# Optimization experiments

Hardware: AMD Instinct MI355X
Metric: run time of the kernel (lower is better)

## Reference

```python
import jax, jax.numpy as jnp
import numpy as np

NUM_HEADS = 16
HEAD_DIM = 64
NEG_INF = -1000000000.0


def rotary_embedding(x, seq_len, head_dim):
    # x: (batch, seq, heads, head_dim)
    positions = jnp.arange(seq_len)
    dim_pairs = jnp.arange(0, head_dim, 2)
    freqs = 1.0 / 10000.0 ** (dim_pairs / head_dim)
    angles = positions[:, None] * freqs[None, :]          # (seq, head_dim/2)
    cos = jnp.cos(angles)[:, None, :]                     # (seq, 1, head_dim/2) -> broadcast over heads
    sin = jnp.sin(angles)[:, None, :]
    x1 = x[..., ::2]
    x2 = x[..., 1::2]
    out1 = x1 * cos - x2 * sin
    out2 = x1 * sin + x2 * cos
    return jnp.stack([out1, out2], axis=-1).reshape(x.shape)


def setup_inputs() -> dict:
    key = jax.random.key(0)
    k1, k2, k3 = jax.random.split(key, 3)
    batch, seq_len, embed_dim = 2, 2048, 1024
    x = jax.random.normal(k1, (batch, seq_len, embed_dim), dtype=jnp.float32)
    W_qkv = jax.random.normal(k2, (embed_dim, 3 * NUM_HEADS * HEAD_DIM), dtype=jnp.float32) * 0.02
    W_out = jax.random.normal(k3, (NUM_HEADS * HEAD_DIM, embed_dim), dtype=jnp.float32) * 0.02
    return {"x": x, "W_qkv": W_qkv, "W_out": W_out}


def reference(x, W_qkv, W_out):
    batch, seq_len, embed_dim = x.shape
    qkv = jnp.einsum('bse,ef->bsf', x, W_qkv)
    qkv = qkv.reshape(batch, seq_len, 3, NUM_HEADS, HEAD_DIM)
    q, k, v = qkv[:, :, 0], qkv[:, :, 1], qkv[:, :, 2]
    q = rotary_embedding(q, seq_len, HEAD_DIM)
    k = rotary_embedding(k, seq_len, HEAD_DIM)
    scale = 1.0 / jnp.sqrt(jnp.asarray(HEAD_DIM, dtype=x.dtype))
    scores = jnp.einsum('bqhd,bkhd->bhqk', q, k) * scale   # (B,H,S,S)
    mask = jnp.tril(jnp.ones((seq_len, seq_len), dtype=bool))[None, None, :, :]
    scores = jnp.where(mask, scores, NEG_INF)
    weights = jax.nn.softmax(scores, axis=-1)
    out = jnp.einsum('bhqk,bkhd->bqhd', weights, v)
    out = out.reshape(batch, seq_len, NUM_HEADS * HEAD_DIM)
    return jnp.einsum('bsf,fe->bse', out, W_out)
```

## Files before the change

kernel.cpp:

```cpp
#include <hip/hip_runtime.h>
#include <hip/hip_bf16.h>

typedef __attribute__((ext_vector_type(8))) short short8;
typedef __attribute__((ext_vector_type(4))) float float4v;

__global__ __launch_bounds__(256) void cvt_f32_bf16(
    const float* __restrict__ in, __hip_bfloat16* __restrict__ out, int n4) {
  const int i = blockIdx.x * 256 + threadIdx.x;
  if (i >= n4) return;
  const float4 v = *(const float4*)(in + (size_t)i * 4);
  __hip_bfloat16 o[4];
  o[0] = __float2bfloat16(v.x); o[1] = __float2bfloat16(v.y);
  o[2] = __float2bfloat16(v.z); o[3] = __float2bfloat16(v.w);
  *(uint2*)(out + (size_t)i * 4) = *(const uint2*)o;
}

__global__ __launch_bounds__(256) void transpose_f32_bf16(
    const float* __restrict__ in, __hip_bfloat16* __restrict__ out,
    int R, int C) {
  __shared__ __hip_bfloat16 tile[32][33];
  const int c0 = blockIdx.x * 32, r0 = blockIdx.y * 32;
  const int tx = threadIdx.x & 31, ty = threadIdx.x >> 5;
  #pragma unroll
  for (int i = ty; i < 32; i += 8)
    tile[i][tx] = __float2bfloat16(in[(size_t)(r0 + i) * C + (c0 + tx)]);
  __syncthreads();
  #pragma unroll
  for (int i = ty; i < 32; i += 8)
    out[(size_t)(c0 + i) * R + (r0 + tx)] = tile[tx][i];
}

template <typename OutT>
__global__ __launch_bounds__(256) void gemm_bt(
    const __hip_bfloat16* __restrict__ A,
    const __hip_bfloat16* __restrict__ Bt,
    OutT* __restrict__ C,
    int M, int N, int K) {
  __shared__ __hip_bfloat16 lA[128][64];
  __shared__ __hip_bfloat16 lB[128][64];
  const int t = threadIdx.x;
  const int lane = t & 63, wave = t >> 6;
  const int quad = lane >> 4, ln = lane & 15;
  const int m0 = blockIdx.y * 128, n0 = blockIdx.x * 128;
  const int wm = (wave >> 1) * 64, wn = (wave & 1) * 64;
  const int srow = lane >> 3;
  const int schunk = ((lane & 7) ^ srow) * 8;

  float4v acc[4][4];
  #pragma unroll
  for (int i = 0; i < 4; ++i)
    #pragma unroll
    for (int j = 0; j < 4; ++j)
      acc[i][j] = (float4v){0.f, 0.f, 0.f, 0.f};

  for (int kt = 0; kt < K; kt += 64) {
    __syncthreads();
    #pragma unroll
    for (int q = 0; q < 4; ++q) {
      const int rbase = wave * 32 + q * 8;
      __builtin_amdgcn_global_load_lds(
          (const __attribute__((address_space(1))) void*)
              (A + (size_t)(m0 + rbase + srow) * K + kt + schunk),
          (__attribute__((address_space(3))) void*)&lA[rbase][0], 16, 0, 0);
      __builtin_amdgcn_global_load_lds(
          (const __attribute__((address_space(1))) void*)
              (Bt + (size_t)(n0 + rbase + srow) * K + kt + schunk),
          (__attribute__((address_space(3))) void*)&lB[rbase][0], 16, 0, 0);
    }
    __syncthreads();
    #pragma unroll
    for (int step = 0; step < 2; ++step) {
      short8 af[4], bf[4];
      #pragma unroll
      for (int i = 0; i < 4; ++i)
        af[i] = *(const short8*)&lA[wm + i * 16 + ln][((step * 4 + quad) ^ (ln & 7)) * 8];
      #pragma unroll
      for (int j = 0; j < 4; ++j)
        bf[j] = *(const short8*)&lB[wn + j * 16 + ln][((step * 4 + quad) ^ (ln & 7)) * 8];
      #pragma unroll
      for (int i = 0; i < 4; ++i)
        #pragma unroll
        for (int j = 0; j < 4; ++j)
          acc[i][j] = __builtin_amdgcn_mfma_f32_16x16x32_bf16(af[i], bf[j], acc[i][j], 0, 0, 0);
    }
  }
  #pragma unroll
  for (int i = 0; i < 4; ++i)
    #pragma unroll
    for (int j = 0; j < 4; ++j)
      #pragma unroll
      for (int r = 0; r < 4; ++r) {
        const int row = m0 + wm + i * 16 + quad * 4 + r;
        const int col = n0 + wn + j * 16 + ln;
        if constexpr (__is_same(OutT, float))
          C[(size_t)row * N + col] = acc[i][j][r];
        else
          C[(size_t)row * N + col] = __float2bfloat16(acc[i][j][r]);
      }
}

__global__ __launch_bounds__(512) void rope_reshape(
    const __hip_bfloat16* __restrict__ qkv,
    __hip_bfloat16* __restrict__ Q,
    __hip_bfloat16* __restrict__ K) {
  const int row = blockIdx.x;
  const int s = row & 2047;
  const int b = row >> 11;
  const int t = threadIdx.x;
  const int h = t >> 5, pr = t & 31;
  const int d0 = pr * 2;
  const float freq = powf(10000.f, -(float)d0 / 64.f);
  const float ang = (float)s * freq;
  float sn, cs;
  sincosf(ang, &sn, &cs);

  const size_t in_base = (size_t)row * 3072;
  const size_t o = (((size_t)(b * 16 + h)) * 2048 + s) * 64 + d0;

  __hip_bfloat162 q2 = *(const __hip_bfloat162*)&qkv[in_base + h * 64 + d0];
  float x1 = __bfloat162float(q2.x), x2 = __bfloat162float(q2.y);
  __hip_bfloat162 qo;
  qo.x = __float2bfloat16((x1 * cs - x2 * sn) * 0.125f);
  qo.y = __float2bfloat16((x1 * sn + x2 * cs) * 0.125f);
  *(__hip_bfloat162*)&Q[o] = qo;

  __hip_bfloat162 k2 = *(const __hip_bfloat162*)&qkv[in_base + 1024 + h * 64 + d0];
  x1 = __bfloat162float(k2.x); x2 = __bfloat162float(k2.y);
  __hip_bfloat162 ko;
  ko.x = __float2bfloat16(x1 * cs - x2 * sn);
  ko.y = __float2bfloat16(x1 * sn + x2 * cs);
  *(__hip_bfloat162*)&K[o] = ko;
}

__global__ __launch_bounds__(256) void v_transpose(
    const __hip_bfloat16* __restrict__ qkv,
    __hip_bfloat16* __restrict__ Vt) {
  __shared__ __hip_bfloat16 tile[64][65];
  const int bh = blockIdx.y;
  const int h = bh & 15, b = bh >> 4;
  const int s0 = blockIdx.x * 64;
  const int tx = threadIdx.x & 63, ty = threadIdx.x >> 6;
  #pragma unroll
  for (int i = ty; i < 64; i += 4)
    tile[i][tx] = qkv[(size_t)(b * 2048 + s0 + i) * 3072 + 2048 + h * 64 + tx];
  __syncthreads();
  #pragma unroll
  for (int i = ty; i < 64; i += 4)
    Vt[((size_t)bh * 64 + i) * 2048 + s0 + tx] = tile[tx][i];
}

__global__ __launch_bounds__(256) void attention(
    const __hip_bfloat16* __restrict__ Q,
    const __hip_bfloat16* __restrict__ K,
    const __hip_bfloat16* __restrict__ Vt,
    __hip_bfloat16* __restrict__ attn) {
  __shared__ __hip_bfloat16 lK[2][64][64];
  __shared__ __hip_bfloat16 lV[2][64][64];
  __shared__ __hip_bfloat16 lP[4][16][72];
  const int t = threadIdx.x;
  const int lane = t & 63, w = t >> 6;
  const int quad = lane >> 4, ln = lane & 15;
  const int bh = blockIdx.x;
  const int pair = blockIdx.y;
  const size_t base = (size_t)bh * 2048 * 64;
  const __hip_bfloat16* Qb = Q + base;
  const __hip_bfloat16* Kb = K + base;
  const __hip_bfloat16* Vb = Vt + base;
  const int b = bh >> 4, h = bh & 15;

  short8 ones;
  #pragma unroll
  for (int i = 0; i < 8; ++i) ones[i] = (short)0x3F80;

  const int srow = lane >> 3;
  const int schunk = ((lane & 7) ^ srow) * 8;
  const int rb0 = w * 16;

  #pragma unroll
  for (int ph = 0; ph < 2; ++ph) {
    const int qt = (ph == 0) ? pair : 31 - pair;
    const int q0 = qt * 64;

    __syncthreads();

    #pragma unroll
    for (int g = 0; g < 2; ++g) {
      const int rbase = rb0 + g * 8;
      __builtin_amdgcn_global_load_lds(
          (const __attribute__((address_space(1))) void*)
              (Kb + (size_t)(rbase + srow) * 64 + schunk),
          (__attribute__((address_space(3))) void*)&lK[0][rbase][0], 16, 0, 0);
      __builtin_amdgcn_global_load_lds(
          (const __attribute__((address_space(1))) void*)
              (Vb + (size_t)(rbase + srow) * 2048 + schunk),
          (__attribute__((address_space(3))) void*)&lV[0][rbase][0], 16, 0, 0);
    }

    short8 qf[2];
    {
      const size_t qrow = (size_t)(q0 + w * 16 + ln) * 64;
      qf[0] = *(const short8*)(Qb + qrow + quad * 8);
      qf[1] = *(const short8*)(Qb + qrow + 32 + quad * 8);
    }

    float4v acc_o[4];
    #pragma unroll
    for (int dt = 0; dt < 4; ++dt) acc_o[dt] = (float4v){0.f, 0.f, 0.f, 0.f};
    float4v acc_l = (float4v){0.f, 0.f, 0.f, 0.f};

    for (int kt = 0; kt <= qt; ++kt) {
      const int buf = kt & 1;
      __syncthreads();

      if (kt < qt) {
        #pragma unroll
        for (int g = 0; g < 2; ++g) {
          const int rbase = rb0 + g * 8;
          __builtin_amdgcn_global_load_lds(
              (const __attribute__((address_space(1))) void*)
                  (Kb + (size_t)((kt + 1) * 64 + rbase + srow) * 64 + schunk),
              (__attribute__((address_space(3))) void*)&lK[buf ^ 1][rbase][0], 16, 0, 0);
          __builtin_amdgcn_global_load_lds(
              (const __attribute__((address_space(1))) void*)
                  (Vb + (size_t)(rbase + srow) * 2048 + (kt + 1) * 64 + schunk),
              (__attribute__((address_space(3))) void*)&lV[buf ^ 1][rbase][0], 16, 0, 0);
        }
      }

      float4v s4[4];
      #pragma unroll
      for (int nt = 0; nt < 4; ++nt) {
        float4v a = (float4v){0.f, 0.f, 0.f, 0.f};
        #pragma unroll
        for (int step = 0; step < 2; ++step) {
          short8 kf = *(const short8*)&lK[buf][nt * 16 + ln][((step * 4 + quad) ^ (ln & 7)) * 8];
          a = __builtin_amdgcn_mfma_f32_16x16x32_bf16(qf[step], kf, a, 0, 0, 0);
        }
        s4[nt] = a;
      }
      if (kt == qt) {
        #pragma unroll
        for (int nt = 0; nt < 4; ++nt)
          #pragma unroll
          for (int r = 0; r < 4; ++r) {
            const int sk = kt * 64 + nt * 16 + ln;
            const int qr = q0 + w * 16 + quad * 4 + r;
            if (sk > qr) s4[nt][r] = -64.f;
          }
      }
      #pragma unroll
      for (int nt = 0; nt < 4; ++nt)
        #pragma unroll
        for (int r = 0; r < 4; ++r)
          lP[w][quad * 4 + r][nt * 16 + ln] = __float2bfloat16(__expf(s4[nt][r]));
      #pragma unroll
      for (int step = 0; step < 2; ++step) {
        short8 pf = *(const short8*)&lP[w][ln][step * 32 + quad * 8];
        acc_l = __builtin_amdgcn_mfma_f32_16x16x32_bf16(pf, ones, acc_l, 0, 0, 0);
        #pragma unroll
        for (int dt = 0; dt < 4; ++dt) {
          short8 vf = *(const short8*)&lV[buf][dt * 16 + ln][((step * 4 + quad) ^ (ln & 7)) * 8];
          acc_o[dt] = __builtin_amdgcn_mfma_f32_16x16x32_bf16(pf, vf, acc_o[dt], 0, 0, 0);
        }
      }
    }

    float inv_l[4];
    #pragma unroll
    for (int r = 0; r < 4; ++r) inv_l[r] = 1.0f / acc_l[r];
    #pragma unroll
    for (int dt = 0; dt < 4; ++dt)
      #pragma unroll
      for (int r = 0; r < 4; ++r) {
        const int qr = q0 + w * 16 + quad * 4 + r;
        const size_t rg = (size_t)(b * 2048 + qr);
        const int col = h * 64 + dt * 16 + ln;
        attn[rg * 1024 + col] = __float2bfloat16(acc_o[dt][r] * inv_l[r]);
      }
  }
}

extern "C" void kernel_launch(void* const* d_in, const int* in_sizes, int n_in,
                              void* d_out, int out_size, void* d_ws, size_t ws_size,
                              hipStream_t stream) {
  const float* x    = (const float*)d_in[0];
  const float* Wqkv = (const float*)d_in[1];
  const float* Wout = (const float*)d_in[2];
  float* out = (float*)d_out;

  __hip_bfloat16* ws = (__hip_bfloat16*)d_ws;
  __hip_bfloat16* xb    = ws;
  __hip_bfloat16* WqkvT = xb    + (size_t)4096 * 1024;
  __hip_bfloat16* WoutT = WqkvT + (size_t)3072 * 1024;
  __hip_bfloat16* qkv   = WoutT + (size_t)1024 * 1024;
  __hip_bfloat16* Q     = qkv   + (size_t)4096 * 3072;
  __hip_bfloat16* K     = Q     + (size_t)32 * 2048 * 64;
  __hip_bfloat16* Vt    = K     + (size_t)32 * 2048 * 64;
  __hip_bfloat16* attn  = Vt    + (size_t)32 * 2048 * 64;

  cvt_f32_bf16<<<4096, 256, 0, stream>>>(x, xb, 4096 * 1024 / 4);
  transpose_f32_bf16<<<dim3(3072 / 32, 1024 / 32), 256, 0, stream>>>(Wqkv, WqkvT, 1024, 3072);
  transpose_f32_bf16<<<dim3(1024 / 32, 1024 / 32), 256, 0, stream>>>(Wout, WoutT, 1024, 1024);
  gemm_bt<__hip_bfloat16><<<dim3(3072 / 128, 4096 / 128), 256, 0, stream>>>(xb, WqkvT, qkv, 4096, 3072, 1024);
  rope_reshape<<<4096, 512, 0, stream>>>(qkv, Q, K);
  v_transpose<<<dim3(32, 32), 256, 0, stream>>>(qkv, Vt);
  attention<<<dim3(32, 16), 256, 0, stream>>>(Q, K, Vt, attn);
  gemm_bt<float><<<dim3(1024 / 128, 4096 / 128), 256, 0, stream>>>(attn, WoutT, out, 4096, 1024, 1024);
}
```

Baseline: 199.4 us.

## Split attention into per-tile blocks, fuse RoPE with V transpose, narrow output GEMM tile

Attention now launches one block per (head, query tile), 1024 blocks ordered heaviest-first, in place of paired tiles in 512 blocks. This is meant to improve load balance and occupancy. RoPE and the V transpose are merged into one kernel, saving a launch and a pass over qkv. Q is pre-scaled by log2(e) so the softmax can use exp2f. The output GEMM uses 128x64 tiles to double its block count, at the cost of less operand reuse per block.

```diff
diff --git a/kernel.cpp b/kernel.cpp
--- a/kernel.cpp
+++ b/kernel.cpp
@@ -30,27 +30,28 @@
     out[(size_t)(c0 + i) * R + (r0 + tx)] = tile[tx][i];
 }
 
-template <typename OutT>
+template <typename OutT, int BN>
 __global__ __launch_bounds__(256) void gemm_bt(
     const __hip_bfloat16* __restrict__ A,
     const __hip_bfloat16* __restrict__ Bt,
     OutT* __restrict__ C,
     int M, int N, int K) {
   __shared__ __hip_bfloat16 lA[128][64];
-  __shared__ __hip_bfloat16 lB[128][64];
+  __shared__ __hip_bfloat16 lB[BN][64];
+  constexpr int NJ = BN / 32;
   const int t = threadIdx.x;
   const int lane = t & 63, wave = t >> 6;
   const int quad = lane >> 4, ln = lane & 15;
-  const int m0 = blockIdx.y * 128, n0 = blockIdx.x * 128;
-  const int wm = (wave >> 1) * 64, wn = (wave & 1) * 64;
+  const int m0 = blockIdx.y * 128, n0 = blockIdx.x * BN;
+  const int wm = (wave >> 1) * 64, wn = (wave & 1) * (BN / 2);
   const int srow = lane >> 3;
   const int schunk = ((lane & 7) ^ srow) * 8;
 
-  float4v acc[4][4];
+  float4v acc[4][NJ];
   #pragma unroll
   for (int i = 0; i < 4; ++i)
     #pragma unroll
-    for (int j = 0; j < 4; ++j)
+    for (int j = 0; j < NJ; ++j)
       acc[i][j] = (float4v){0.f, 0.f, 0.f, 0.f};
 
   for (int kt = 0; kt < K; kt += 64) {
@@ -62,6 +63,10 @@
           (const __attribute__((address_space(1))) void*)
               (A + (size_t)(m0 + rbase + srow) * K + kt + schunk),
           (__attribute__((address_space(3))) void*)&lA[rbase][0], 16, 0, 0);
+    }
+    #pragma unroll
+    for (int g = 0; g < BN / 32; ++g) {
+      const int rbase = wave * (BN / 4) + g * 8;
       __builtin_amdgcn_global_load_lds(
           (const __attribute__((address_space(1))) void*)
               (Bt + (size_t)(n0 + rbase + srow) * K + kt + schunk),
@@ -70,24 +75,24 @@
     __syncthreads();
     #pragma unroll
     for (int step = 0; step < 2; ++step) {
-      short8 af[4], bf[4];
+      short8 af[4], bf[NJ];
       #pragma unroll
       for (int i = 0; i < 4; ++i)
         af[i] = *(const short8*)&lA[wm + i * 16 + ln][((step * 4 + quad) ^ (ln & 7)) * 8];
       #pragma unroll
-      for (int j = 0; j < 4; ++j)
+      for (int j = 0; j < NJ; ++j)
         bf[j] = *(const short8*)&lB[wn + j * 16 + ln][((step * 4 + quad) ^ (ln & 7)) * 8];
       #pragma unroll
       for (int i = 0; i < 4; ++i)
         #pragma unroll
-        for (int j = 0; j < 4; ++j)
+        for (int j = 0; j < NJ; ++j)
           acc[i][j] = __builtin_amdgcn_mfma_f32_16x16x32_bf16(af[i], bf[j], acc[i][j], 0, 0, 0);
     }
   }
   #pragma unroll
   for (int i = 0; i < 4; ++i)
     #pragma unroll
-    for (int j = 0; j < 4; ++j)
+    for (int j = 0; j < NJ; ++j)
       #pragma unroll
       for (int r = 0; r < 4; ++r) {
         const int row = m0 + wm + i * 16 + quad * 4 + r;
@@ -99,47 +104,45 @@
       }
 }
 
-__global__ __launch_bounds__(512) void rope_reshape(
+__global__ __launch_bounds__(256) void qkv_prep(
     const __hip_bfloat16* __restrict__ qkv,
     __hip_bfloat16* __restrict__ Q,
-    __hip_bfloat16* __restrict__ K) {
-  const int row = blockIdx.x;
-  const int s = row & 2047;
-  const int b = row >> 11;
+    __hip_bfloat16* __restrict__ K,
+    __hip_bfloat16* __restrict__ Vt) {
+  __shared__ __hip_bfloat16 tile[64][65];
+  const int s0 = blockIdx.x * 64;
+  const int bh = blockIdx.y;
+  const int h = bh & 15, b = bh >> 4;
   const int t = threadIdx.x;
-  const int h = t >> 5, pr = t & 31;
+
+  const int pr = t & 31, sl = t >> 5;
   const int d0 = pr * 2;
   const float freq = powf(10000.f, -(float)d0 / 64.f);
-  const float ang = (float)s * freq;
-  float sn, cs;
-  sincosf(ang, &sn, &cs);
-
-  const size_t in_base = (size_t)row * 3072;
-  const size_t o = (((size_t)(b * 16 + h)) * 2048 + s) * 64 + d0;
-
-  __hip_bfloat162 q2 = *(const __hip_bfloat162*)&qkv[in_base + h * 64 + d0];
-  float x1 = __bfloat162float(q2.x), x2 = __bfloat162float(q2.y);
-  __hip_bfloat162 qo;
-  qo.x = __float2bfloat16((x1 * cs - x2 * sn) * 0.125f);
-  qo.y = __float2bfloat16((x1 * sn + x2 * cs) * 0.125f);
-  *(__hip_bfloat162*)&Q[o] = qo;
-
-  __hip_bfloat162 k2 = *(const __hip_bfloat162*)&qkv[in_base + 1024 + h * 64 + d0];
-  x1 = __bfloat162float(k2.x); x2 = __bfloat162float(k2.y);
-  __hip_bfloat162 ko;
-  ko.x = __float2bfloat16(x1 * cs - x2 * sn);
-  ko.y = __float2bfloat16(x1 * sn + x2 * cs);
-  *(__hip_bfloat162*)&K[o] = ko;
-}
-
-__global__ __launch_bounds__(256) void v_transpose(
-    const __hip_bfloat16* __restrict__ qkv,
-    __hip_bfloat16* __restrict__ Vt) {
-  __shared__ __hip_bfloat16 tile[64][65];
-  const int bh = blockIdx.y;
-  const int h = bh & 15, b = bh >> 4;
-  const int s0 = blockIdx.x * 64;
-  const int tx = threadIdx.x & 63, ty = threadIdx.x >> 6;
+  const float qs = 0.125f * 1.44269504088896340736f;
+  #pragma unroll
+  for (int ss = sl; ss < 64; ss += 8) {
+    const int s = s0 + ss;
+    float sn, cs;
+    sincosf((float)s * freq, &sn, &cs);
+    const size_t in_base = (size_t)(b * 2048 + s) * 3072;
+    const size_t o = ((size_t)bh * 2048 + s) * 64 + d0;
+
+    __hip_bfloat162 q2 = *(const __hip_bfloat162*)&qkv[in_base + h * 64 + d0];
+    float x1 = __bfloat162float(q2.x), x2 = __bfloat162float(q2.y);
+    __hip_bfloat162 qo;
+    qo.x = __float2bfloat16((x1 * cs - x2 * sn) * qs);
+    qo.y = __float2bfloat16((x1 * sn + x2 * cs) * qs);
+    *(__hip_bfloat162*)&Q[o] = qo;
+
+    __hip_bfloat162 k2 = *(const __hip_bfloat162*)&qkv[in_base + 1024 + h * 64 + d0];
+    x1 = __bfloat162float(k2.x); x2 = __bfloat162float(k2.y);
+    __hip_bfloat162 ko;
+    ko.x = __float2bfloat16(x1 * cs - x2 * sn);
+    ko.y = __float2bfloat16(x1 * sn + x2 * cs);
+    *(__hip_bfloat162*)&K[o] = ko;
+  }
+
+  const int tx = t & 63, ty = t >> 6;
   #pragma unroll
   for (int i = ty; i < 64; i += 4)
     tile[i][tx] = qkv[(size_t)(b * 2048 + s0 + i) * 3072 + 2048 + h * 64 + tx];
@@ -160,8 +163,10 @@
   const int t = threadIdx.x;
   const int lane = t & 63, w = t >> 6;
   const int quad = lane >> 4, ln = lane & 15;
-  const int bh = blockIdx.x;
-  const int pair = blockIdx.y;
+  const int id = blockIdx.x;
+  const int bh = id & 31;
+  const int qt = 31 - (id >> 5);
+  const int q0 = qt * 64;
   const size_t base = (size_t)bh * 2048 * 64;
   const __hip_bfloat16* Qb = Q + base;
   const __hip_bfloat16* Kb = K + base;
@@ -177,107 +182,99 @@
   const int rb0 = w * 16;
 
   #pragma unroll
-  for (int ph = 0; ph < 2; ++ph) {
-    const int qt = (ph == 0) ? pair : 31 - pair;
-    const int q0 = qt * 64;
-
+  for (int g = 0; g < 2; ++g) {
+    const int rbase = rb0 + g * 8;
+    __builtin_amdgcn_global_load_lds(
+        (const __attribute__((address_space(1))) void*)
+            (Kb + (size_t)(rbase + srow) * 64 + schunk),
+        (__attribute__((address_space(3))) void*)&lK[0][rbase][0], 16, 0, 0);
+    __builtin_amdgcn_global_load_lds(
+        (const __attribute__((address_space(1))) void*)
+            (Vb + (size_t)(rbase + srow) * 2048 + schunk),
+        (__attribute__((address_space(3))) void*)&lV[0][rbase][0], 16, 0, 0);
+  }
+
+  short8 qf[2];
+  {
+    const size_t qrow = (size_t)(q0 + w * 16 + ln) * 64;
+    qf[0] = *(const short8*)(Qb + qrow + quad * 8);
+    qf[1] = *(const short8*)(Qb + qrow + 32 + quad * 8);
+  }
+
+  float4v acc_o[4];
+  #pragma unroll
+  for (int dt = 0; dt < 4; ++dt) acc_o[dt] = (float4v){0.f, 0.f, 0.f, 0.f};
+  float4v acc_l = (float4v){0.f, 0.f, 0.f, 0.f};
+
+  for (int kt = 0; kt <= qt; ++kt) {
+    const int buf = kt & 1;
     __syncthreads();
 
-    #pragma unroll
-    for (int g = 0; g < 2; ++g) {
-      const int rbase = rb0 + g * 8;
-      __builtin_amdgcn_global_load_lds(
-          (const __attribute__((address_space(1))) void*)
-              (Kb + (size_t)(rbase + srow) * 64 + schunk),
-          (__attribute__((address_space(3))) void*)&lK[0][rbase][0], 16, 0, 0);
-      __builtin_amdgcn_global_load_lds(
-          (const __attribute__((address_space(1))) void*)
-              (Vb + (size_t)(rbase + srow) * 2048 + schunk),
-          (__attribute__((address_space(3))) void*)&lV[0][rbase][0], 16, 0, 0);
-    }
-
-    short8 qf[2];
-    {
-      const size_t qrow = (size_t)(q0 + w * 16 + ln) * 64;
-      qf[0] = *(const short8*)(Qb + qrow + quad * 8);
-      qf[1] = *(const short8*)(Qb + qrow + 32 + quad * 8);
-    }
-
-    float4v acc_o[4];
-    #pragma unroll
-    for (int dt = 0; dt < 4; ++dt) acc_o[dt] = (float4v){0.f, 0.f, 0.f, 0.f};
-    float4v acc_l = (float4v){0.f, 0.f, 0.f, 0.f};
-
-    for (int kt = 0; kt <= qt; ++kt) {
-      const int buf = kt & 1;
-      __syncthreads();
-
-      if (kt < qt) {
-        #pragma unroll
-        for (int g = 0; g < 2; ++g) {
-          const int rbase = rb0 + g * 8;
-          __builtin_amdgcn_global_load_lds(
-              (const __attribute__((address_space(1))) void*)
-                  (Kb + (size_t)((kt + 1) * 64 + rbase + srow) * 64 + schunk),
-              (__attribute__((address_space(3))) void*)&lK[buf ^ 1][rbase][0], 16, 0, 0);
-          __builtin_amdgcn_global_load_lds(
-              (const __attribute__((address_space(1))) void*)
-                  (Vb + (size_t)(rbase + srow) * 2048 + (kt + 1) * 64 + schunk),
-              (__attribute__((address_space(3))) void*)&lV[buf ^ 1][rbase][0], 16, 0, 0);
-        }
+    if (kt < qt) {
+      #pragma unroll
+      for (int g = 0; g < 2; ++g) {
+        const int rbase = rb0 + g * 8;
+        __builtin_amdgcn_global_load_lds(
+            (const __attribute__((address_space(1))) void*)
+                (Kb + (size_t)((kt + 1) * 64 + rbase + srow) * 64 + schunk),
+            (__attribute__((address_space(3))) void*)&lK[buf ^ 1][rbase][0], 16, 0, 0);
+        __builtin_amdgcn_global_load_lds(
+            (const __attribute__((address_space(1))) void*)
+                (Vb + (size_t)(rbase + srow) * 2048 + (kt + 1) * 64 + schunk),
+            (__attribute__((address_space(3))) void*)&lV[buf ^ 1][rbase][0], 16, 0, 0);
       }
-
-      float4v s4[4];
-      #pragma unroll
-      for (int nt = 0; nt < 4; ++nt) {
-        float4v a = (float4v){0.f, 0.f, 0.f, 0.f};
-        #pragma unroll
-        for (int step = 0; step < 2; ++step) {
-          short8 kf = *(const short8*)&lK[buf][nt * 16 + ln][((step * 4 + quad) ^ (ln & 7)) * 8];
-          a = __builtin_amdgcn_mfma_f32_16x16x32_bf16(qf[step], kf, a, 0, 0, 0);
-        }
-        s4[nt] = a;
+    }
+
+    float4v s4[4];
+    #pragma unroll
+    for (int nt = 0; nt < 4; ++nt) {
+      float4v a = (float4v){0.f, 0.f, 0.f, 0.f};
+      #pragma unroll
+      for (int step = 0; step < 2; ++step) {
+        short8 kf = *(const short8*)&lK[buf][nt * 16 + ln][((step * 4 + quad) ^ (ln & 7)) * 8];
+        a = __builtin_amdgcn_mfma_f32_16x16x32_bf16(qf[step], kf, a, 0, 0, 0);
       }
-      if (kt == qt) {
-        #pragma unroll
-        for (int nt = 0; nt < 4; ++nt)
-          #pragma unroll
-          for (int r = 0; r < 4; ++r) {
-            const int sk = kt * 64 + nt * 16 + ln;
-            const int qr = q0 + w * 16 + quad * 4 + r;
-            if (sk > qr) s4[nt][r] = -64.f;
-          }
-      }
+      s4[nt] = a;
+    }
+    if (kt == qt) {
       #pragma unroll
       for (int nt = 0; nt < 4; ++nt)
         #pragma unroll
-        for (int r = 0; r < 4; ++r)
-          lP[w][quad * 4 + r][nt * 16 + ln] = __float2bfloat16(__expf(s4[nt][r]));
-      #pragma unroll
-      for (int step = 0; step < 2; ++step) {
-        short8 pf = *(const short8*)&lP[w][ln][step * 32 + quad * 8];
-        acc_l = __builtin_amdgcn_mfma_f32_16x16x32_bf16(pf, ones, acc_l, 0, 0, 0);
-        #pragma unroll
-        for (int dt = 0; dt < 4; ++dt) {
-          short8 vf = *(const short8*)&lV[buf][dt * 16 + ln][((step * 4 + quad) ^ (ln & 7)) * 8];
-          acc_o[dt] = __builtin_amdgcn_mfma_f32_16x16x32_bf16(pf, vf, acc_o[dt], 0, 0, 0);
+        for (int r = 0; r < 4; ++r) {
+          const int sk = kt * 64 + nt * 16 + ln;
+          const int qr = q0 + w * 16 + quad * 4 + r;
+          if (sk > qr) s4[nt][r] = -64.f;
         }
+    }
+    #pragma unroll
+    for (int nt = 0; nt < 4; ++nt)
+      #pragma unroll
+      for (int r = 0; r < 4; ++r)
+        lP[w][quad * 4 + r][nt * 16 + ln] = __float2bfloat16(exp2f(s4[nt][r]));
+    #pragma unroll
+    for (int step = 0; step < 2; ++step) {
+      short8 pf = *(const short8*)&lP[w][ln][step * 32 + quad * 8];
+      acc_l = __builtin_amdgcn_mfma_f32_16x16x32_bf16(pf, ones, acc_l, 0, 0, 0);
+      #pragma unroll
+      for (int dt = 0; dt < 4; ++dt) {
+        short8 vf = *(const short8*)&lV[buf][dt * 16 + ln][((step * 4 + quad) ^ (ln & 7)) * 8];
+        acc_o[dt] = __builtin_amdgcn_mfma_f32_16x16x32_bf16(pf, vf, acc_o[dt], 0, 0, 0);
       }
     }
-
-    float inv_l[4];
-    #pragma unroll
-    for (int r = 0; r < 4; ++r) inv_l[r] = 1.0f / acc_l[r];
-    #pragma unroll
-    for (int dt = 0; dt < 4; ++dt)
-      #pragma unroll
-      for (int r = 0; r < 4; ++r) {
-        const int qr = q0 + w * 16 + quad * 4 + r;
-        const size_t rg = (size_t)(b * 2048 + qr);
-        const int col = h * 64 + dt * 16 + ln;
-        attn[rg * 1024 + col] = __float2bfloat16(acc_o[dt][r] * inv_l[r]);
-      }
-  }
+  }
+
+  float inv_l[4];
+  #pragma unroll
+  for (int r = 0; r < 4; ++r) inv_l[r] = 1.0f / acc_l[r];
+  #pragma unroll
+  for (int dt = 0; dt < 4; ++dt)
+    #pragma unroll
+    for (int r = 0; r < 4; ++r) {
+      const int qr = q0 + w * 16 + quad * 4 + r;
+      const size_t rg = (size_t)(b * 2048 + qr);
+      const int col = h * 64 + dt * 16 + ln;
+      attn[rg * 1024 + col] = __float2bfloat16(acc_o[dt][r] * inv_l[r]);
+    }
 }
 
 extern "C" void kernel_launch(void* const* d_in, const int* in_sizes, int n_in,
@@ -301,9 +298,8 @@
   cvt_f32_bf16<<<4096, 256, 0, stream>>>(x, xb, 4096 * 1024 / 4);
   transpose_f32_bf16<<<dim3(3072 / 32, 1024 / 32), 256, 0, stream>>>(Wqkv, WqkvT, 1024, 3072);
   transpose_f32_bf16<<<dim3(1024 / 32, 1024 / 32), 256, 0, stream>>>(Wout, WoutT, 1024, 1024);
-  gemm_bt<__hip_bfloat16><<<dim3(3072 / 128, 4096 / 128), 256, 0, stream>>>(xb, WqkvT, qkv, 4096, 3072, 1024);
-  rope_reshape<<<4096, 512, 0, stream>>>(qkv, Q, K);
-  v_transpose<<<dim3(32, 32), 256, 0, stream>>>(qkv, Vt);
-  attention<<<dim3(32, 16), 256, 0, stream>>>(Q, K, Vt, attn);
-  gemm_bt<float><<<dim3(1024 / 128, 4096 / 128), 256, 0, stream>>>(attn, WoutT, out, 4096, 1024, 1024);
-}
+  gemm_bt<__hip_bfloat16, 128><<<dim3(3072 / 128, 4096 / 128), 256, 0, stream>>>(xb, WqkvT, qkv, 4096, 3072, 1024);
+  qkv_prep<<<dim3(32, 32), 256, 0, stream>>>(qkv, Q, K, Vt);
+  attention<<<1024, 256, 0, stream>>>(Q, K, Vt, attn);
+  gemm_bt<float, 64><<<dim3(1024 / 64, 4096 / 128), 256, 0, stream>>>(attn, WoutT, out, 4096, 1024, 1024);
+}
```

Result: faster. 191.1 us (-4.2%).
